# Performance work log

Hardware: AMD Instinct MI355X
Metric: run time of the kernel (lower is better)

Reference implementation:

```python
import jax, jax.numpy as jnp
import numpy as np

B, T, C = 64, 256, 384
H = 6
D = C // H  # head_size = 64


def setup_inputs() -> dict:
    key = jax.random.key(0)
    ks = jax.random.split(key, 6)
    s = 1.0 / np.sqrt(C)
    return {
        "x": jax.random.normal(ks[0], (B, T, C), dtype=jnp.float32),
        "Wk": jax.random.uniform(ks[1], (C, C), jnp.float32, -s, s),
        "Wq": jax.random.uniform(ks[2], (C, C), jnp.float32, -s, s),
        "Wv": jax.random.uniform(ks[3], (C, C), jnp.float32, -s, s),
        "Wo": jax.random.uniform(ks[4], (C, C), jnp.float32, -s, s),
        "bo": jax.random.uniform(ks[5], (C,), jnp.float32, -s, s),
    }


def reference(x, Wk, Wq, Wv, Wo, bo):
    b, t, c = x.shape
    # QKV projections (no bias), split heads: [B, H, T, D]
    k = (x @ Wk.T).reshape(b, t, H, D).transpose(0, 2, 1, 3)
    q = (x @ Wq.T).reshape(b, t, H, D).transpose(0, 2, 1, 3)
    v = (x @ Wv.T).reshape(b, t, H, D).transpose(0, 2, 1, 3)
    # Scores scaled by C**-0.5 (as in the original module, not head_size**-0.5)
    wei = jnp.einsum("bhqd,bhkd->bhqk", q, k) * (c ** -0.5)
    mask = jnp.tril(jnp.ones((t, t), dtype=bool))
    wei = jnp.where(mask, wei, -jnp.inf)
    wei = jax.nn.softmax(wei, axis=-1)
    out = jnp.einsum("bhqk,bhkd->bhqd", wei, v)
    out = out.transpose(0, 2, 1, 3).reshape(b, t, c)
    # Output projection (dropout is identity at inference)
    return out @ Wo.T + bo
```

## Files before the change

kernel.cpp:

```cpp
#include <hip/hip_runtime.h>
#include <hip/hip_bf16.h>

typedef unsigned short u16;
typedef __attribute__((ext_vector_type(8))) short short8;
typedef __attribute__((ext_vector_type(4))) float f32x4;

#define BATCH 64
#define SEQ   256
#define CDIM  384
#define NHEAD 6
#define DHEAD 64
#define NROW  16384

constexpr float SCALE = 0.051031036307982884f;

__device__ __forceinline__ f32x4 mfma16(short8 a, short8 b, f32x4 c) {
    return __builtin_amdgcn_mfma_f32_16x16x32_bf16(a, b, c, 0, 0, 0);
}

__device__ __forceinline__ u16 f2b(float f) {
    __hip_bfloat16 h = __float2bfloat16(f);
    return *reinterpret_cast<u16*>(&h);
}

__device__ __forceinline__ void gload_lds16(const u16* g, u16* l) {
    __builtin_amdgcn_global_load_lds(
        (const __attribute__((address_space(1))) void*)g,
        (__attribute__((address_space(3))) void*)l, 16, 0, 0);
}

__global__ __launch_bounds__(256) void cvt_all(
        const float* __restrict__ x,
        const float* __restrict__ Wk, const float* __restrict__ Wq,
        const float* __restrict__ Wv, const float* __restrict__ Wo,
        u16* __restrict__ xb,
        u16* __restrict__ wkb, u16* __restrict__ wqb,
        u16* __restrict__ wvb, u16* __restrict__ wob)
{
    int blk = blockIdx.x;
    const float* s;
    u16* d;
    if (blk < 3072) {
        s = x; d = xb;
    } else {
        const int w = blk - 3072;
        const int z = w / 72;
        blk = w - z * 72;
        s = (z == 0) ? Wk : (z == 1) ? Wq : (z == 2) ? Wv : Wo;
        d = (z == 0) ? wkb : (z == 1) ? wqb : (z == 2) ? wvb : wob;
    }
    const int i = (blk * 256 + (int)threadIdx.x) * 8;
    const float4 a = *(const float4*)(s + i);
    const float4 b = *(const float4*)(s + i + 4);
    short8 r;
    r[0] = (short)f2b(a.x); r[1] = (short)f2b(a.y);
    r[2] = (short)f2b(a.z); r[3] = (short)f2b(a.w);
    r[4] = (short)f2b(b.x); r[5] = (short)f2b(b.y);
    r[6] = (short)f2b(b.z); r[7] = (short)f2b(b.w);
    *(short8*)(d + i) = r;
}

__global__ __launch_bounds__(256) void gemm_qkv(
        const u16* __restrict__ X, const u16* __restrict__ Wk,
        const u16* __restrict__ Wv, const u16* __restrict__ Wq,
        u16* __restrict__ Kd, u16* __restrict__ VTd, u16* __restrict__ Qd)
{
    __shared__ u16 SMEM[17408];

    const int bid   = blockIdx.x;
    const int xcd   = bid & 7;
    const int i     = bid >> 3;
    const int igrp  = i / 9;
    const int j     = i - igrp * 9;
    const int panel = xcd * 16 + igrp;
    const int m0    = panel * 128;
    const int n0    = (j % 3) * 128;
    const int z     = j / 3;
    const u16* W = (z == 0) ? Wk : (z == 1 ? Wv : Wq);

    const int tid  = threadIdx.x;
    const int lane = tid & 63;
    const int wv   = tid >> 6;
    const int l15  = lane & 15;
    const int q4   = lane >> 4;
    const int wm   = (wv >> 1) * 64;
    const int wn   = (wv & 1) * 64;

    f32x4 acc[4][4] = {};

    auto STAGE = [&](int kk, int buf) {
#pragma unroll
        for (int ch = 0; ch < 4; ++ch) {
            const int half = ch & 1;
            const int f = (half * 256 + tid) * 8;
            const int r = f >> 5;
            const int c = f & 31;
            const int ci = c ^ (((r >> 1) & 3) << 3);
            u16* dst = SMEM + buf * 8192 + (ch < 2 ? 0 : 4096)
                     + (half * 256 + wv * 64) * 8;
            if (ch < 2)
                gload_lds16(X + (size_t)(m0 + r) * CDIM + kk + ci, dst);
            else
                gload_lds16(W + (size_t)(n0 + r) * CDIM + kk + ci, dst);
        }
    };

    STAGE(0, 0);
#pragma unroll
    for (int t = 0; t < 12; ++t) {
        const int cur = t & 1;
        if (t < 11) {
            STAGE((t + 1) * 32, cur ^ 1);
            asm volatile("s_waitcnt vmcnt(4)" ::: "memory");
        } else {
            asm volatile("s_waitcnt vmcnt(0)" ::: "memory");
        }
        asm volatile("s_barrier" ::: "memory");

        const u16* As = SMEM + cur * 8192;
        const u16* Bs = As + 4096;
        short8 af[4], bf[4];
#pragma unroll
        for (int tt = 0; tt < 4; ++tt) {
            const int ra = wm + tt * 16 + l15;
            const int rb = wn + tt * 16 + l15;
            af[tt] = *(const short8*)(As + ra * 32 +
                    ((q4 * 8) ^ (((ra >> 1) & 3) << 3)));
            bf[tt] = *(const short8*)(Bs + rb * 32 +
                    ((q4 * 8) ^ (((rb >> 1) & 3) << 3)));
        }
#pragma unroll
        for (int tm = 0; tm < 4; ++tm)
#pragma unroll
            for (int tn = 0; tn < 4; ++tn)
                acc[tm][tn] = mfma16(af[tm], bf[tn], acc[tm][tn]);

        asm volatile("s_barrier" ::: "memory");
    }

    if (z != 1) {
        u16* D = (z == 0) ? Kd : Qd;
        u16* T = SMEM;
#pragma unroll
        for (int tm = 0; tm < 4; ++tm)
#pragma unroll
            for (int tn = 0; tn < 4; ++tn) {
                const int cl = wn + tn * 16 + l15;
#pragma unroll
                for (int r = 0; r < 4; ++r) {
                    const int row = wm + tm * 16 + q4 * 4 + r;
                    T[row * 128 + (((cl >> 3) ^ (row & 7)) << 3) + (cl & 7)] =
                        f2b(acc[tm][tn][r]);
                }
            }
        __syncthreads();
        const int seg0 = tid >> 3;
        const int c    = tid & 7;
#pragma unroll
        for (int it = 0; it < 8; ++it) {
            const int S   = it * 32 + seg0;
            const int row = S >> 1;
            const int hf  = S & 1;
            const int rowg = m0 + row;
            const int b  = rowg >> 8, tt = rowg & 255;
            const int h  = (n0 + hf * 64) >> 6;
            const int chunk = (hf * 8 + c) ^ (row & 7);
            *(uint4*)(D + (size_t)((b * NHEAD + h) * SEQ + tt) * DHEAD + c * 8) =
                *(const uint4*)(T + row * 128 + chunk * 8);
        }
    } else {
        u16* T = SMEM;
#pragma unroll
        for (int tm = 0; tm < 4; ++tm)
#pragma unroll
            for (int tn = 0; tn < 4; ++tn) {
                const int cl = wn + tn * 16 + l15;
#pragma unroll
                for (int r = 0; r < 4; ++r) {
                    const int rl = wm + tm * 16 + q4 * 4 + r;
                    T[cl * 136 + rl] = f2b(acc[tm][tn][r]);
                }
            }
        __syncthreads();
        const int b  = m0 >> 8;
        const int t0 = m0 & 255;
        const int fl = tid >> 1;
        const int hf = tid & 1;
        const int fg = n0 + fl;
        const int h  = fg >> 6, d = fg & 63;
        u16* dst = VTd + ((size_t)(b * NHEAD + h) * DHEAD + d) * SEQ + t0 + hf * 64;
        const u16* src = T + fl * 136 + hf * 64;
#pragma unroll
        for (int j2 = 0; j2 < 8; ++j2)
            *(uint4*)(dst + j2 * 8) = *(const uint4*)(src + j2 * 8);
    }
}

#define PLD 136

template <int CH>
__device__ __forceinline__ void attn_body(
        const u16* __restrict__ Qg, const u16* __restrict__ Kg,
        const u16* __restrict__ VTg, u16* __restrict__ Og, int bh,
        u16* SA, u16* Pbase)
{
    constexpr int NKEY = 64 * (CH + 1);
    constexpr int KT   = NKEY / 16;
    constexpr int NPH  = (NKEY + 127) / 128;
    constexpr int R0   = (NKEY < 128) ? NKEY : 128;
    constexpr int R1   = NKEY - R0;

    const int tid  = threadIdx.x;
    const int wv   = tid >> 6;
    const int lane = tid & 63;
    const int l15  = lane & 15;
    const int q4   = lane >> 4;
    const int qrow0 = CH * 64 + wv * 16;
    const int qmax  = qrow0 + 15;
    u16* Pl = Pbase + wv * 16 * PLD;

    short8 aq[2];
#pragma unroll
    for (int ks = 0; ks < 2; ++ks)
        aq[ks] = *(const short8*)(Qg + (size_t)(bh * SEQ + qrow0 + l15) * DHEAD
                                     + ks * 32 + q4 * 8);

    u16* Kbuf = SA;
    f32x4 s[KT];
#pragma unroll
    for (int ph = 0; ph < NPH; ++ph) {
        const int rows = (NKEY - ph * 128) < 128 ? (NKEY - ph * 128) : 128;
        for (int it = 0; it < rows / 32; ++it) {
            const int r  = it * 32 + (tid >> 3);
            const int d0 = (tid & 7) * 8;
            *(uint4*)(Kbuf + r * 72 + d0) =
                *(const uint4*)(Kg + (size_t)(bh * SEQ + ph * 128 + r) * DHEAD + d0);
        }
        __syncthreads();
#pragma unroll
        for (int t = 0; t < rows / 16; ++t) {
            const int gt = ph * 8 + t;
            if (gt * 16 <= qmax) {
                f32x4 z = {0.f, 0.f, 0.f, 0.f};
#pragma unroll
                for (int ks = 0; ks < 2; ++ks) {
                    short8 bk = *(const short8*)(Kbuf + (t * 16 + l15) * 72
                                                 + ks * 32 + q4 * 8);
                    z = mfma16(aq[ks], bk, z);
                }
                const int kc = gt * 16 + l15;
#pragma unroll
                for (int r = 0; r < 4; ++r) {
                    float v = z[r] * SCALE;
                    if (kc > qrow0 + q4 * 4 + r) v = -1e30f;
                    z[r] = v;
                }
                s[gt] = z;
            } else {
                f32x4 neg = {-1e30f, -1e30f, -1e30f, -1e30f};
                s[gt] = neg;
            }
        }
        __syncthreads();
    }

    float mx[4], sm[4], rs[4];
#pragma unroll
    for (int r = 0; r < 4; ++r) {
        float m = -1e30f;
#pragma unroll
        for (int t = 0; t < KT; ++t) m = fmaxf(m, s[t][r]);
#pragma unroll
        for (int off = 1; off < 16; off <<= 1)
            m = fmaxf(m, __shfl_xor(m, off, 16));
        mx[r] = m;
        sm[r] = 0.f;
    }
#pragma unroll
    for (int t = 0; t < KT; ++t)
#pragma unroll
        for (int r = 0; r < 4; ++r) {
            float p = __expf(s[t][r] - mx[r]);
            s[t][r] = p;
            sm[r] += p;
        }
#pragma unroll
    for (int r = 0; r < 4; ++r) {
#pragma unroll
        for (int off = 1; off < 16; off <<= 1)
            sm[r] += __shfl_xor(sm[r], off, 16);
        rs[r] = 1.f / sm[r];
    }

    u16* Vt = SA;
    f32x4 o[4] = {};

    constexpr int C0  = R0 >> 3;
    constexpr int NV0 = (64 * C0) / 256;
#pragma unroll
    for (int it = 0; it < NV0; ++it) {
        const int flat = it * 256 + tid;
        const int rd = flat / C0;
        const int kc = (flat - rd * C0) * 8;
        *(uint4*)(Vt + rd * 136 + kc) =
            *(const uint4*)(VTg + ((size_t)bh * DHEAD + rd) * SEQ + kc);
    }
#pragma unroll
    for (int gt = 0; gt < R0 / 16; ++gt)
#pragma unroll
        for (int r = 0; r < 4; ++r)
            Pl[(q4 * 4 + r) * PLD + gt * 16 + l15] = f2b(s[gt][r]);
    __syncthreads();

#pragma unroll
    for (int ks = 0; ks < R0 / 32; ++ks) {
        if (ks * 32 <= qmax) {
            short8 ap = *(const short8*)(Pl + l15 * PLD + ks * 32 + q4 * 8);
#pragma unroll
            for (int tn = 0; tn < 4; ++tn) {
                short8 bv = *(const short8*)(Vt + (tn * 16 + l15) * 136
                                             + ks * 32 + q4 * 8);
                o[tn] = mfma16(ap, bv, o[tn]);
            }
        }
    }

    if constexpr (NPH == 2) {
        __syncthreads();
        constexpr int C1  = R1 >> 3;
        constexpr int NV1 = (64 * C1) / 256;
#pragma unroll
        for (int it = 0; it < NV1; ++it) {
            const int flat = it * 256 + tid;
            const int rd = flat / C1;
            const int kc = (flat - rd * C1) * 8;
            *(uint4*)(Vt + rd * 136 + kc) =
                *(const uint4*)(VTg + ((size_t)bh * DHEAD + rd) * SEQ + 128 + kc);
        }
#pragma unroll
        for (int gt = 8; gt < KT; ++gt)
#pragma unroll
            for (int r = 0; r < 4; ++r)
                Pl[(q4 * 4 + r) * PLD + (gt - 8) * 16 + l15] = f2b(s[gt][r]);
        __syncthreads();

#pragma unroll
        for (int ks = 0; ks < R1 / 32; ++ks) {
            const int gks = 4 + ks;
            if (gks * 32 <= qmax) {
                short8 ap = *(const short8*)(Pl + l15 * PLD + ks * 32 + q4 * 8);
#pragma unroll
                for (int tn = 0; tn < 4; ++tn) {
                    short8 bv = *(const short8*)(Vt + (tn * 16 + l15) * 136
                                                 + ks * 32 + q4 * 8);
                    o[tn] = mfma16(ap, bv, o[tn]);
                }
            }
        }
    }
    __syncthreads();

    u16* OL = SA;
#pragma unroll
    for (int tn = 0; tn < 4; ++tn) {
        const int col = tn * 16 + l15;
#pragma unroll
        for (int r = 0; r < 4; ++r) {
            const int row = wv * 16 + q4 * 4 + r;
            OL[row * 64 + (((col >> 3) ^ (row & 7)) << 3) + (col & 7)] =
                f2b(o[tn][r] * rs[r]);
        }
    }
    __syncthreads();
    const int b  = bh / NHEAD;
    const int h  = bh - b * NHEAD;
    const int seg0 = tid >> 3;
    const int c    = tid & 7;
#pragma unroll
    for (int it = 0; it < 2; ++it) {
        const int row = it * 32 + seg0;
        const int chunk = c ^ (row & 7);
        *(uint4*)(Og + (size_t)(b * SEQ + CH * 64 + row) * CDIM
                     + h * DHEAD + c * 8) =
            *(const uint4*)(OL + row * 64 + chunk * 8);
    }
}

__global__ __launch_bounds__(256, 4) void attn_kernel(
        const u16* __restrict__ Qg, const u16* __restrict__ Kg,
        const u16* __restrict__ VTg, u16* __restrict__ Og)
{
    __shared__ u16 SA[128 * 72];
    __shared__ u16 Pls[4 * 16 * PLD];
    const int bid = blockIdx.x;
    const int xcd = bid & 7;
    const int g   = bid >> 3;
    const int bh  = xcd * 48 + (g >> 2);
    const int ch  = g & 3;
    switch (ch) {
        case 0: attn_body<0>(Qg, Kg, VTg, Og, bh, SA, Pls); break;
        case 1: attn_body<1>(Qg, Kg, VTg, Og, bh, SA, Pls); break;
        case 2: attn_body<2>(Qg, Kg, VTg, Og, bh, SA, Pls); break;
        default: attn_body<3>(Qg, Kg, VTg, Og, bh, SA, Pls); break;
    }
}

__global__ __launch_bounds__(256) void gemm_out(
        const u16* __restrict__ O, const u16* __restrict__ Wo,
        const float* __restrict__ bias, float* __restrict__ out)
{
    __shared__ u16 As[64 * 64];
    __shared__ u16 Bs[128 * 64];

    const int bid = blockIdx.x;
    const int xcd = bid & 7;
    const int g   = bid >> 3;
    const int mt  = xcd * 32 + g / 3;
    const int n0  = (g % 3) * 128;
    const int m0  = mt * 64;

    const int tid  = threadIdx.x;
    const int lane = tid & 63;
    const int wv   = tid >> 6;
    const int l15  = lane & 15;
    const int q4   = lane >> 4;
    const int wm   = (wv >> 1) * 32;
    const int wn   = (wv & 1) * 64;

    f32x4 acc[2][4] = {};

    for (int kk = 0; kk < CDIM; kk += 64) {
        __syncthreads();
#pragma unroll
        for (int ch = 0; ch < 4; ++ch) {
            const int f = (ch * 256 + tid) * 8;
            const int r = f >> 6;
            const int c = (f ^ ((r & 7) << 3)) & 63;
            const int lb = (ch * 256 + wv * 64) * 8;
            gload_lds16(Wo + (size_t)(n0 + r) * CDIM + kk + c, Bs + lb);
            if (ch < 2)
                gload_lds16(O + (size_t)(m0 + r) * CDIM + kk + c, As + lb);
        }
        __syncthreads();

#pragma unroll
        for (int ks = 0; ks < 2; ++ks) {
            short8 af[2], bf[4];
#pragma unroll
            for (int t = 0; t < 2; ++t) {
                const int ra = wm + t * 16 + l15;
                af[t] = *(const short8*)(As + ra * 64 +
                        ((ks * 32 + q4 * 8) ^ ((ra & 7) << 3)));
            }
#pragma unroll
            for (int t = 0; t < 4; ++t) {
                const int rb = wn + t * 16 + l15;
                bf[t] = *(const short8*)(Bs + rb * 64 +
                        ((ks * 32 + q4 * 8) ^ ((rb & 7) << 3)));
            }
#pragma unroll
            for (int tm = 0; tm < 2; ++tm)
#pragma unroll
                for (int tn = 0; tn < 4; ++tn)
                    acc[tm][tn] = mfma16(af[tm], bf[tn], acc[tm][tn]);
        }
    }

#pragma unroll
    for (int tm = 0; tm < 2; ++tm) {
#pragma unroll
        for (int tn = 0; tn < 4; ++tn) {
            const int col = n0 + wn + tn * 16 + l15;
            const float bb = bias[col];
#pragma unroll
            for (int r = 0; r < 4; ++r) {
                const int row = m0 + wm + tm * 16 + q4 * 4 + r;
                out[(size_t)row * CDIM + col] = acc[tm][tn][r] + bb;
            }
        }
    }
}

extern "C" void kernel_launch(void* const* d_in, const int* in_sizes, int n_in,
                              void* d_out, int out_size, void* d_ws, size_t ws_size,
                              hipStream_t stream)
{
    const float* x  = (const float*)d_in[0];
    const float* Wk = (const float*)d_in[1];
    const float* Wq = (const float*)d_in[2];
    const float* Wv = (const float*)d_in[3];
    const float* Wo = (const float*)d_in[4];
    const float* bo = (const float*)d_in[5];
    float* out = (float*)d_out;

    const size_t SZ = (size_t)NROW * CDIM;
    const size_t WZ = (size_t)CDIM * CDIM;
    u16* xb  = (u16*)d_ws;
    u16* Wkb = xb  + SZ;
    u16* Wqb = Wkb + WZ;
    u16* Wvb = Wqb + WZ;
    u16* Wob = Wvb + WZ;
    u16* Kw  = Wob + WZ;
    u16* Qw  = Kw + SZ;
    u16* Ow  = Qw + SZ;
    u16* VTw = (u16*)d_out;

    cvt_all<<<dim3(3360), 256, 0, stream>>>(
        x, Wk, Wq, Wv, Wo, xb, Wkb, Wqb, Wvb, Wob);

    gemm_qkv<<<dim3(1152), 256, 0, stream>>>(xb, Wkb, Wvb, Wqb, Kw, VTw, Qw);

    attn_kernel<<<dim3(1536), 256, 0, stream>>>(Qw, Kw, VTw, Ow);

    gemm_out<<<dim3(768), 256, 0, stream>>>(Ow, Wob, bo, out);
}
```

Before: 138.2 us.

## Fuse fp32-to-bf16 conversion of x into QKV GEMM tile loads

The separate conversion pass over the activation x is dropped. The QKV GEMM now streams fp32 x tiles straight into LDS with a new XOR swizzle and packs them to bf16 in registers before the MFMAs, while only the weights are still pre-converted. This removes a full write and re-read of the bf16 copy of x and one kernel's worth of x traffic. In exchange, each of the 9 blocks sharing a row panel loads twice the bytes of x, LDS use grows from 34 KB to 48 KB (which may lower occupancy), and the inner loop does extra conversion work.

```diff
diff --git a/kernel.cpp b/kernel.cpp
--- a/kernel.cpp
+++ b/kernel.cpp
@@ -23,49 +23,43 @@
     return *reinterpret_cast<u16*>(&h);
 }
 
-__device__ __forceinline__ void gload_lds16(const u16* g, u16* l) {
-    __builtin_amdgcn_global_load_lds(
-        (const __attribute__((address_space(1))) void*)g,
-        (__attribute__((address_space(3))) void*)l, 16, 0, 0);
-}
-
-__global__ __launch_bounds__(256) void cvt_all(
-        const float* __restrict__ x,
-        const float* __restrict__ Wk, const float* __restrict__ Wq,
-        const float* __restrict__ Wv, const float* __restrict__ Wo,
-        u16* __restrict__ xb,
-        u16* __restrict__ wkb, u16* __restrict__ wqb,
-        u16* __restrict__ wvb, u16* __restrict__ wob)
-{
-    int blk = blockIdx.x;
-    const float* s;
-    u16* d;
-    if (blk < 3072) {
-        s = x; d = xb;
-    } else {
-        const int w = blk - 3072;
-        const int z = w / 72;
-        blk = w - z * 72;
-        s = (z == 0) ? Wk : (z == 1) ? Wq : (z == 2) ? Wv : Wo;
-        d = (z == 0) ? wkb : (z == 1) ? wqb : (z == 2) ? wvb : wob;
-    }
-    const int i = (blk * 256 + (int)threadIdx.x) * 8;
-    const float4 a = *(const float4*)(s + i);
-    const float4 b = *(const float4*)(s + i + 4);
+__device__ __forceinline__ short8 pack8(float4 a, float4 b) {
     short8 r;
     r[0] = (short)f2b(a.x); r[1] = (short)f2b(a.y);
     r[2] = (short)f2b(a.z); r[3] = (short)f2b(a.w);
     r[4] = (short)f2b(b.x); r[5] = (short)f2b(b.y);
     r[6] = (short)f2b(b.z); r[7] = (short)f2b(b.w);
-    *(short8*)(d + i) = r;
+    return r;
+}
+
+__device__ __forceinline__ void gload_lds16(const void* g, u16* l) {
+    __builtin_amdgcn_global_load_lds(
+        (const __attribute__((address_space(1))) void*)g,
+        (__attribute__((address_space(3))) void*)l, 16, 0, 0);
+}
+
+__global__ __launch_bounds__(256) void cvt_w(
+        const float* __restrict__ Wk, const float* __restrict__ Wq,
+        const float* __restrict__ Wv, const float* __restrict__ Wo,
+        u16* __restrict__ wkb, u16* __restrict__ wqb,
+        u16* __restrict__ wvb, u16* __restrict__ wob)
+{
+    const int z   = blockIdx.x / 72;
+    const int blk = blockIdx.x - z * 72;
+    const float* s = (z == 0) ? Wk : (z == 1) ? Wq : (z == 2) ? Wv : Wo;
+    u16*         d = (z == 0) ? wkb : (z == 1) ? wqb : (z == 2) ? wvb : wob;
+    const int i = (blk * 256 + (int)threadIdx.x) * 8;
+    const float4 a = *(const float4*)(s + i);
+    const float4 b = *(const float4*)(s + i + 4);
+    *(short8*)(d + i) = pack8(a, b);
 }
 
 __global__ __launch_bounds__(256) void gemm_qkv(
-        const u16* __restrict__ X, const u16* __restrict__ Wk,
+        const float* __restrict__ X, const u16* __restrict__ Wk,
         const u16* __restrict__ Wv, const u16* __restrict__ Wq,
         u16* __restrict__ Kd, u16* __restrict__ VTd, u16* __restrict__ Qd)
 {
-    __shared__ u16 SMEM[17408];
+    __shared__ u16 SMEM[24576];
 
     const int bid   = blockIdx.x;
     const int xcd   = bid & 7;
@@ -90,18 +84,21 @@
 
     auto STAGE = [&](int kk, int buf) {
 #pragma unroll
-        for (int ch = 0; ch < 4; ++ch) {
-            const int half = ch & 1;
-            const int f = (half * 256 + tid) * 8;
+        for (int it = 0; it < 4; ++it) {
+            const int fc = it * 256 + tid;
+            const int r  = fc >> 3;
+            const int cs = (fc & 7) ^ (r & 7);
+            gload_lds16(X + (size_t)(m0 + r) * CDIM + kk + cs * 4,
+                        SMEM + buf * 12288 + (it * 256 + wv * 64) * 8);
+        }
+#pragma unroll
+        for (int ch = 0; ch < 2; ++ch) {
+            const int f = (ch * 256 + tid) * 8;
             const int r = f >> 5;
             const int c = f & 31;
             const int ci = c ^ (((r >> 1) & 3) << 3);
-            u16* dst = SMEM + buf * 8192 + (ch < 2 ? 0 : 4096)
-                     + (half * 256 + wv * 64) * 8;
-            if (ch < 2)
-                gload_lds16(X + (size_t)(m0 + r) * CDIM + kk + ci, dst);
-            else
-                gload_lds16(W + (size_t)(n0 + r) * CDIM + kk + ci, dst);
+            gload_lds16(W + (size_t)(n0 + r) * CDIM + kk + ci,
+                        SMEM + buf * 12288 + 8192 + (ch * 256 + wv * 64) * 8);
         }
     };
 
@@ -111,21 +108,24 @@
         const int cur = t & 1;
         if (t < 11) {
             STAGE((t + 1) * 32, cur ^ 1);
-            asm volatile("s_waitcnt vmcnt(4)" ::: "memory");
+            asm volatile("s_waitcnt vmcnt(6)" ::: "memory");
         } else {
             asm volatile("s_waitcnt vmcnt(0)" ::: "memory");
         }
         asm volatile("s_barrier" ::: "memory");
 
-        const u16* As = SMEM + cur * 8192;
-        const u16* Bs = As + 4096;
+        const u16* As = SMEM + cur * 12288;
+        const u16* Bs = As + 8192;
         short8 af[4], bf[4];
 #pragma unroll
         for (int tt = 0; tt < 4; ++tt) {
             const int ra = wm + tt * 16 + l15;
+            const float4 lo = *(const float4*)(As + ra * 64 +
+                    (((2 * q4) ^ (ra & 7)) << 3));
+            const float4 hi = *(const float4*)(As + ra * 64 +
+                    (((2 * q4 + 1) ^ (ra & 7)) << 3));
+            af[tt] = pack8(lo, hi);
             const int rb = wn + tt * 16 + l15;
-            af[tt] = *(const short8*)(As + ra * 32 +
-                    ((q4 * 8) ^ (((ra >> 1) & 3) << 3)));
             bf[tt] = *(const short8*)(Bs + rb * 32 +
                     ((q4 * 8) ^ (((rb >> 1) & 3) << 3)));
         }
@@ -495,8 +495,7 @@
 
     const size_t SZ = (size_t)NROW * CDIM;
     const size_t WZ = (size_t)CDIM * CDIM;
-    u16* xb  = (u16*)d_ws;
-    u16* Wkb = xb  + SZ;
+    u16* Wkb = (u16*)d_ws;
     u16* Wqb = Wkb + WZ;
     u16* Wvb = Wqb + WZ;
     u16* Wob = Wvb + WZ;
@@ -505,10 +504,10 @@
     u16* Ow  = Qw + SZ;
     u16* VTw = (u16*)d_out;
 
-    cvt_all<<<dim3(3360), 256, 0, stream>>>(
-        x, Wk, Wq, Wv, Wo, xb, Wkb, Wqb, Wvb, Wob);
-
-    gemm_qkv<<<dim3(1152), 256, 0, stream>>>(xb, Wkb, Wvb, Wqb, Kw, VTw, Qw);
+    cvt_w<<<dim3(288), 256, 0, stream>>>(
+        Wk, Wq, Wv, Wo, Wkb, Wqb, Wvb, Wob);
+
+    gemm_qkv<<<dim3(1152), 256, 0, stream>>>(x, Wkb, Wvb, Wqb, Kw, VTw, Qw);
 
     attn_kernel<<<dim3(1536), 256, 0, stream>>>(Qw, Kw, VTw, Ow);
 
```

Result: slower. 145.1 us (+5.0%).
